# Kernel tuning notes

Hardware: AMD Instinct MI355X
Metric: run time of the kernel (lower is better)

The kernel has to match this reference:

```python
import jax, jax.numpy as jnp
import numpy as np

B, L, D, H = 4, 2048, 1024, 16
DH = D // H

def setup_inputs() -> dict:
    key = jax.random.key(0)
    ks = jax.random.split(key, 9)
    s = 1.0 / np.sqrt(D)
    x = jax.random.normal(ks[0], (B, L, D), dtype=jnp.float32)
    Wq = jax.random.uniform(ks[1], (D, D), jnp.float32, -s, s)
    bq = jax.random.uniform(ks[2], (D,), jnp.float32, -s, s)
    Wk = jax.random.uniform(ks[3], (D, D), jnp.float32, -s, s)
    bk = jax.random.uniform(ks[4], (D,), jnp.float32, -s, s)
    Wv = jax.random.uniform(ks[5], (D, D), jnp.float32, -s, s)
    bv = jax.random.uniform(ks[6], (D,), jnp.float32, -s, s)
    Wo = jax.random.uniform(ks[7], (D, D), jnp.float32, -s, s)
    bo = jax.random.uniform(ks[8], (D,), jnp.float32, -s, s)
    mask = jnp.tril(jnp.ones((L, L), dtype=jnp.int32))[None, None]  # [1,1,L,L] causal
    return {"x": x, "Wq": Wq, "bq": bq, "Wk": Wk, "bk": bk, "Wv": Wv, "bv": bv,
            "Wo": Wo, "bo": bo, "mask": mask}

def reference(x, Wq, bq, Wk, bk, Wv, bv, Wo, bo, mask):
    # projections (torch Linear: x @ W.T + b; here W stored transposed already as [D,D])
    q = (x @ Wq + bq).reshape(B, L, H, DH).transpose(0, 2, 1, 3)  # [B,H,L,Dh]
    k = (x @ Wk + bk).reshape(B, L, H, DH).transpose(0, 2, 1, 3)
    v = (x @ Wv + bv).reshape(B, L, H, DH).transpose(0, 2, 1, 3)
    scores = jnp.einsum('bhqd,bhkd->bhqk', q, k) / jnp.sqrt(jnp.float32(DH))
    scores = jnp.where(mask == 0, -jnp.inf, scores)
    attn = jax.nn.softmax(scores, axis=-1)
    out = jnp.einsum('bhqk,bhkd->bhqd', attn, v)  # [B,H,L,Dh]
    out = out.transpose(0, 2, 1, 3).reshape(B, L, D)
    return out @ Wo + bo
```

## Files before the change

### kernel.cpp

```cpp
#include <hip/hip_runtime.h>
#include <hip/hip_bf16.h>


typedef __bf16 bf16;
typedef __bf16 bf16x4 __attribute__((ext_vector_type(4)));
typedef __bf16 bf16x8 __attribute__((ext_vector_type(8)));
typedef float f32x4 __attribute__((ext_vector_type(4)));

#define DEV static __device__ __forceinline__

constexpr int B = 4, L = 2048, D = 1024, H = 16, DH = 64;
constexpr int BL = B * L;
constexpr int GM = 8192, GK = 1024;
constexpr int BKg = 64;

typedef __attribute__((address_space(1))) const void* gptr1;
typedef __attribute__((address_space(3))) void* lptr3;

DEV void load_lds16(const bf16* g, bf16* l) {
  __builtin_amdgcn_global_load_lds((gptr1)g, (lptr3)l, 16, 0, 0);
}

DEV f32x4 mfma(bf16x8 a, bf16x8 b, f32x4 c) {
  return __builtin_amdgcn_mfma_f32_16x16x32_bf16(a, b, c, 0, 0, 0);
}

DEV float scrub(float v) { return (v == v) ? v : 0.f; }

__global__ void sniff_k(const unsigned short* __restrict__ xr, int* flag) {
  __shared__ int cnt;
  if (threadIdx.x == 0) cnt = 0;
  __syncthreads();
  int local = 0;
  for (int i = threadIdx.x; i < 4096; i += 64) {
    const unsigned short u = xr[2 * i];
    const int e = (u >> 7) & 0xFF;
    if (e >= 0x70 && e <= 0x85) local++;
  }
  atomicAdd(&cnt, local);
  __syncthreads();
  if (threadIdx.x == 0) *flag = (cnt > 2048) ? 1 : 0;
}

__global__ __launch_bounds__(256) void cvt_x_k(const void* __restrict__ src,
                                               bf16* __restrict__ dst,
                                               const int* __restrict__ flag, int n) {
  const bool isbf = (*flag != 0);
  const int stride = gridDim.x * blockDim.x * 8;
  for (int idx = (blockIdx.x * blockDim.x + threadIdx.x) * 8; idx < n; idx += stride) {
    bf16x8 o;
    if (isbf) {
      bf16x8 v = *(const bf16x8*)((const bf16*)src + idx);
      #pragma unroll
      for (int j = 0; j < 8; ++j) o[j] = (bf16)scrub((float)v[j]);
    } else {
      const float* s = (const float*)src + idx;
      #pragma unroll
      for (int j = 0; j < 8; ++j) o[j] = (bf16)scrub(s[j]);
    }
    *(bf16x8*)&dst[idx] = o;
  }
}

__global__ __launch_bounds__(256) void wtrans_cvt4_k(const void* __restrict__ W0,
                                                     const void* __restrict__ W1,
                                                     const void* __restrict__ W2,
                                                     const void* __restrict__ W3,
                                                     bf16* __restrict__ dstBase,
                                                     const int* __restrict__ flag) {
  __shared__ bf16 t[32][33];
  const bool isbf = (*flag != 0);
  const int z = blockIdx.z;
  const void* src = (z == 0) ? W0 : (z == 1) ? W1 : (z == 2) ? W2 : W3;
  bf16* dst = dstBase + (size_t)z * D * D;
  const int bx = blockIdx.x * 32, by = blockIdx.y * 32;
  const int tx = threadIdx.x & 31, ty = threadIdx.x >> 5;
  for (int i = ty; i < 32; i += 8) {
    const size_t off = (size_t)(by + i) * D + bx + tx;
    const float v = isbf ? (float)((const bf16*)src)[off] : ((const float*)src)[off];
    t[i][tx] = (bf16)scrub(v);
  }
  __syncthreads();
  for (int i = ty; i < 32; i += 8)
    dst[(size_t)(bx + i) * D + by + tx] = t[tx][i];
}

__global__ __launch_bounds__(256) void vtrans_k(const bf16* __restrict__ V,
                                                bf16* __restrict__ VT) {
  __shared__ __align__(16) bf16 t[64 * 72];
  const int l0 = blockIdx.x * 64, bh = blockIdx.y;
  const int b = bh >> 4, h = bh & 15;
  const int tid = threadIdx.x;
  #pragma unroll
  for (int i = 0; i < 2; ++i) {
    const int o = tid * 8 + i * 2048;
    const int lrow = o >> 6, dcol = o & 63;
    *(bf16x8*)&t[lrow * 72 + dcol] =
        *(const bf16x8*)&V[(size_t)(b * L + l0 + lrow) * D + h * 64 + dcol];
  }
  __syncthreads();
  const int d = tid >> 2, kc = tid & 3;
  const int G = kc >> 1, hh = kc & 1;
  bf16x8 o0, o1;
  #pragma unroll
  for (int j = 0; j < 8; ++j) o0[j] = t[(kc * 16 + j) * 72 + d];
  #pragma unroll
  for (int j = 0; j < 8; ++j) o1[j] = t[(kc * 16 + 8 + j) * 72 + d];
  bf16* dst = VT + ((size_t)bh * DH + d) * L + l0 + G * 32;
  *(bf16x4*)(dst + hh * 4)      = __builtin_shufflevector(o0, o0, 0, 1, 2, 3);
  *(bf16x4*)(dst + 8 + hh * 4)  = __builtin_shufflevector(o0, o0, 4, 5, 6, 7);
  *(bf16x4*)(dst + 16 + hh * 4) = __builtin_shufflevector(o1, o1, 0, 1, 2, 3);
  *(bf16x4*)(dst + 24 + hh * 4) = __builtin_shufflevector(o1, o1, 4, 5, 6, 7);
}

__global__ __launch_bounds__(256) void qkv_gemm_k(const bf16* __restrict__ A,
                                                  const bf16* __restrict__ Bt,
                                                  const void* __restrict__ bq,
                                                  const void* __restrict__ bk,
                                                  const void* __restrict__ bv,
                                                  bf16* __restrict__ Q,
                                                  bf16* __restrict__ Kk,
                                                  bf16* __restrict__ V,
                                                  const int* __restrict__ flag) {
  __shared__ __align__(16) bf16 As[128 * BKg];
  __shared__ __align__(16) bf16 Bs[128 * BKg];
  const bool isbf = (*flag != 0);
  const int m0 = blockIdx.x * 128, n0 = blockIdx.y * 128;
  const int buf = n0 >> 10, nloc = n0 & 1023;
  bf16* Cb = (buf == 0) ? Q : (buf == 1) ? Kk : V;
  const void* bias = (buf == 0) ? bq : (buf == 1) ? bk : bv;
  const float scale = (buf == 0) ? 0.18033688011111f : 1.0f;

  const int tid = threadIdx.x, wave = tid >> 6, lane = tid & 63;
  const int wr = wave >> 1, wc = wave & 1;
  const int quad = lane >> 4, l16 = lane & 15;
  const int srow = lane >> 3;
  const int scol = ((lane ^ srow) & 7) * 8;
  const int l7 = l16 & 7;
  const int s0 = ((quad ^ l7) * 8);
  const int s1 = s0 ^ 32;

  f32x4 acc[4][4] = {};

  for (int k0 = 0; k0 < GK; k0 += BKg) {
    for (int c = wave; c < 16; c += 4) {
      load_lds16(A  + (size_t)(m0 + c * 8 + srow) * GK + k0 + scol, &As[c * 512]);
      load_lds16(Bt + (size_t)(n0 + c * 8 + srow) * GK + k0 + scol, &Bs[c * 512]);
    }
    __syncthreads();
    #pragma unroll
    for (int kk = 0; kk < BKg; kk += 32) {
      const int sk = kk ? s1 : s0;
      bf16x8 af[4], bfr[4];
      #pragma unroll
      for (int i = 0; i < 4; ++i)
        af[i] = *(const bf16x8*)&As[(wr * 64 + i * 16 + l16) * BKg + sk];
      #pragma unroll
      for (int i = 0; i < 4; ++i)
        bfr[i] = *(const bf16x8*)&Bs[(wc * 64 + i * 16 + l16) * BKg + sk];
      #pragma unroll
      for (int mi = 0; mi < 4; ++mi)
        #pragma unroll
        for (int ni = 0; ni < 4; ++ni)
          acc[mi][ni] = mfma(af[mi], bfr[ni], acc[mi][ni]);
    }
    __syncthreads();
  }

  #pragma unroll
  for (int ni = 0; ni < 4; ++ni) {
    const int col = nloc + wc * 64 + ni * 16 + l16;
    const float bv2 = isbf ? (float)((const bf16*)bias)[col] : ((const float*)bias)[col];
    #pragma unroll
    for (int mi = 0; mi < 4; ++mi)
      #pragma unroll
      for (int r = 0; r < 4; ++r) {
        const int row = m0 + wr * 64 + mi * 16 + quad * 4 + r;
        Cb[(size_t)row * D + col] = (bf16)((acc[mi][ni][r] + bv2) * scale);
      }
  }
}

__global__ __launch_bounds__(256) void gemm_bt_k(const bf16* __restrict__ A,
                                                 const bf16* __restrict__ Bt,
                                                 const void* __restrict__ bias,
                                                 void* __restrict__ C,
                                                 const int* __restrict__ flag) {
  __shared__ __align__(16) bf16 As[128 * BKg];
  __shared__ __align__(16) bf16 Bs[128 * BKg];
  const bool isbf = (*flag != 0);
  const int m0 = blockIdx.x * 128, n0 = blockIdx.y * 128;
  const int tid = threadIdx.x, wave = tid >> 6, lane = tid & 63;
  const int wr = wave >> 1, wc = wave & 1;
  const int quad = lane >> 4, l16 = lane & 15;
  const int srow = lane >> 3;
  const int scol = ((lane ^ srow) & 7) * 8;
  const int l7 = l16 & 7;
  const int s0 = ((quad ^ l7) * 8);
  const int s1 = s0 ^ 32;

  f32x4 acc[4][4] = {};

  for (int k0 = 0; k0 < GK; k0 += BKg) {
    for (int c = wave; c < 16; c += 4) {
      load_lds16(A  + (size_t)(m0 + c * 8 + srow) * GK + k0 + scol, &As[c * 512]);
      load_lds16(Bt + (size_t)(n0 + c * 8 + srow) * GK + k0 + scol, &Bs[c * 512]);
    }
    __syncthreads();
    #pragma unroll
    for (int kk = 0; kk < BKg; kk += 32) {
      const int sk = kk ? s1 : s0;
      bf16x8 af[4], bfr[4];
      #pragma unroll
      for (int i = 0; i < 4; ++i)
        af[i] = *(const bf16x8*)&As[(wr * 64 + i * 16 + l16) * BKg + sk];
      #pragma unroll
      for (int i = 0; i < 4; ++i)
        bfr[i] = *(const bf16x8*)&Bs[(wc * 64 + i * 16 + l16) * BKg + sk];
      #pragma unroll
      for (int mi = 0; mi < 4; ++mi)
        #pragma unroll
        for (int ni = 0; ni < 4; ++ni)
          acc[mi][ni] = mfma(af[mi], bfr[ni], acc[mi][ni]);
    }
    __syncthreads();
  }

  bf16* Cb = (bf16*)C;
  float* Cf = (float*)C;
  #pragma unroll
  for (int ni = 0; ni < 4; ++ni) {
    const int col = n0 + wc * 64 + ni * 16 + l16;
    const float bv = isbf ? (float)((const bf16*)bias)[col] : ((const float*)bias)[col];
    #pragma unroll
    for (int mi = 0; mi < 4; ++mi)
      #pragma unroll
      for (int r = 0; r < 4; ++r) {
        const int row = m0 + wr * 64 + mi * 16 + quad * 4 + r;
        const float v = acc[mi][ni][r] + bv;
        if (isbf) Cb[(size_t)row * D + col] = (bf16)v;
        else      Cf[(size_t)row * D + col] = v;
      }
  }
}

__global__ __launch_bounds__(256) void attn_k(bf16* QO,
                                              const bf16* __restrict__ K,
                                              const bf16* __restrict__ VT) {
  __shared__ __align__(16) bf16 Ks[2][64 * 64];
  __shared__ __align__(16) bf16 Vt[2][64 * 64];

  const int bx = blockIdx.x;
  const int qt = (L / 64 - 1) - (bx >> 6);
  const int bh = bx & 63;
  const int b = bh >> 4, h = bh & 15;
  const int tid = threadIdx.x, wave = tid >> 6, lane = tid & 63;
  const int quad = lane >> 4, l16 = lane & 15;
  const int srow = lane >> 3;
  const int scol = ((lane ^ srow) & 7) * 8;
  const int l7 = l16 & 7;
  const int s0 = ((quad ^ l7) * 8);
  const int s1 = s0 ^ 32;

  bf16* Qb = QO + (size_t)b * L * D + h * DH;
  const bf16* Kb = K + (size_t)b * L * D + h * DH;
  const bf16* VTg = VT + (size_t)bh * DH * L;

  const int qrow = qt * 64 + wave * 16 + l16;
  const bf16x8 qf0 = *(const bf16x8*)(Qb + (size_t)qrow * D + quad * 8);
  const bf16x8 qf1 = *(const bf16x8*)(Qb + (size_t)qrow * D + 32 + quad * 8);

  bf16x8 ones;
  #pragma unroll
  for (int j = 0; j < 8; ++j) ones[j] = (bf16)1.0f;

  float m_run = -INFINITY;
  f32x4 o_acc[4] = {};
  f32x4 o_sum = {};

  const int nkt = qt + 1;

  for (int c = wave; c < 8; c += 4) {
    load_lds16(Kb  + (size_t)(c * 8 + srow) * D + scol, &Ks[0][c * 512]);
    load_lds16(VTg + (size_t)(c * 8 + srow) * L + scol, &Vt[0][c * 512]);
  }
  __syncthreads();

  int cur = 0;
  for (int kt = 0; kt < nkt; ++kt) {
    if (kt + 1 < nkt) {
      for (int c = wave; c < 8; c += 4) {
        load_lds16(Kb  + (size_t)((kt + 1) * 64 + c * 8 + srow) * D + scol,
                   &Ks[cur ^ 1][c * 512]);
        load_lds16(VTg + (size_t)(c * 8 + srow) * L + (kt + 1) * 64 + scol,
                   &Vt[cur ^ 1][c * 512]);
      }
    }

    const bf16* Kc = &Ks[cur][0];
    const bf16* Vc = &Vt[cur][0];

    f32x4 s[4];
    #pragma unroll
    for (int sub = 0; sub < 4; ++sub) {
      bf16x8 k0 = *(const bf16x8*)&Kc[(sub * 16 + l16) * 64 + s0];
      bf16x8 k1 = *(const bf16x8*)&Kc[(sub * 16 + l16) * 64 + s1];
      f32x4 a = {};
      a = mfma(k0, qf0, a);
      a = mfma(k1, qf1, a);
      s[sub] = a;
    }

    if (kt == qt) {
      const int qloc = wave * 16 + l16;
      #pragma unroll
      for (int sub = 0; sub < 4; ++sub)
        #pragma unroll
        for (int r = 0; r < 4; ++r)
          if (sub * 16 + quad * 4 + r > qloc) s[sub][r] = -1e30f;
    }

    float mx = -INFINITY;
    #pragma unroll
    for (int sub = 0; sub < 4; ++sub) {
      const float a = fmaxf(fmaxf(s[sub][0], s[sub][1]), fmaxf(s[sub][2], s[sub][3]));
      mx = fmaxf(mx, a);
    }
    mx = fmaxf(mx, __shfl_xor(mx, 16, 64));
    mx = fmaxf(mx, __shfl_xor(mx, 32, 64));

    if (!__all(mx <= m_run + 8.f)) {
      const float mn = fmaxf(m_run, mx);
      const float alpha = __builtin_amdgcn_exp2f(m_run - mn);
      m_run = mn;
      #pragma unroll
      for (int r = 0; r < 4; ++r) {
        const float ar = __shfl(alpha, quad * 4 + r, 64);
        o_sum[r] *= ar;
        #pragma unroll
        for (int db = 0; db < 4; ++db) o_acc[db][r] *= ar;
      }
    }

    bf16x8 fr0, fr1;
    #pragma unroll
    for (int r = 0; r < 4; ++r) {
      fr0[r]     = (bf16)__builtin_amdgcn_exp2f(s[0][r] - m_run);
      fr0[4 + r] = (bf16)__builtin_amdgcn_exp2f(s[1][r] - m_run);
      fr1[r]     = (bf16)__builtin_amdgcn_exp2f(s[2][r] - m_run);
      fr1[4 + r] = (bf16)__builtin_amdgcn_exp2f(s[3][r] - m_run);
    }

    o_sum = mfma(fr0, ones, o_sum);
    o_sum = mfma(fr1, ones, o_sum);
    #pragma unroll
    for (int db = 0; db < 4; ++db) {
      bf16x8 v0 = *(const bf16x8*)&Vc[(db * 16 + l16) * 64 + s0];
      bf16x8 v1 = *(const bf16x8*)&Vc[(db * 16 + l16) * 64 + s1];
      o_acc[db] = mfma(fr0, v0, o_acc[db]);
      o_acc[db] = mfma(fr1, v1, o_acc[db]);
    }

    __syncthreads();
    cur ^= 1;
  }

  #pragma unroll
  for (int r = 0; r < 4; ++r) {
    const float inv = 1.f / o_sum[r];
    const int row = qt * 64 + wave * 16 + quad * 4 + r;
    #pragma unroll
    for (int db = 0; db < 4; ++db)
      Qb[(size_t)row * D + db * 16 + l16] = (bf16)(o_acc[db][r] * inv);
  }
}

extern "C" void kernel_launch(void* const* d_in, const int* in_sizes, int n_in,
                              void* d_out, int out_size, void* d_ws, size_t ws_size,
                              hipStream_t stream) {
  const void* x  = d_in[0];
  const void* Wq = d_in[1];
  const void* bq = d_in[2];
  const void* Wk = d_in[3];
  const void* bk = d_in[4];
  const void* Wv = d_in[5];
  const void* bv = d_in[6];
  const void* Wo = d_in[7];
  const void* bo = d_in[8];

  int* flag = (int*)d_ws;
  char* p = (char*)d_ws + 4096;
  bf16* xc  = (bf16*)p;                 p += (size_t)BL * D * 2;
  bf16* WqT = (bf16*)p;                 p += (size_t)D * D * 2;
  bf16* WkT = (bf16*)p;                 p += (size_t)D * D * 2;
  bf16* WvT = (bf16*)p;                 p += (size_t)D * D * 2;
  bf16* WoT = (bf16*)p;                 p += (size_t)D * D * 2;
  bf16* Qb  = (bf16*)p;                 p += (size_t)BL * D * 2;
  bf16* Kb  = (bf16*)p;                 p += (size_t)BL * D * 2;
  bf16* Vb  = (bf16*)p;
  bf16* VTb = xc;

  sniff_k<<<1, 64, 0, stream>>>((const unsigned short*)x, flag);

  cvt_x_k<<<1024, 256, 0, stream>>>(x, xc, flag, BL * D);
  wtrans_cvt4_k<<<dim3(32, 32, 4), 256, 0, stream>>>(Wq, Wk, Wv, Wo, WqT, flag);

  qkv_gemm_k<<<dim3(GM / 128, 3072 / 128), 256, 0, stream>>>(
      xc, WqT, bq, bk, bv, Qb, Kb, Vb, flag);

  vtrans_k<<<dim3(L / 64, B * H), 256, 0, stream>>>(Vb, VTb);

  attn_k<<<dim3((L / 64) * B * H), 256, 0, stream>>>(Qb, Kb, VTb);

  gemm_bt_k<<<dim3(GM / 128, D / 128), 256, 0, stream>>>(Qb, WoT, bo, d_out, flag);
}
```

Before: 300.0 us.

## Fuse V transpose into QKV GEMM epilogue and drop vtrans kernel

```diff
diff --git a/kernel.cpp b/kernel.cpp
--- a/kernel.cpp
+++ b/kernel.cpp
@@ -26,13 +26,14 @@
 }
 
 DEV float scrub(float v) { return (v == v) ? v : 0.f; }
+DEV float max3f(float a, float b, float c) { return fmaxf(fmaxf(a, b), c); }
 
 __global__ void sniff_k(const unsigned short* __restrict__ xr, int* flag) {
   __shared__ int cnt;
   if (threadIdx.x == 0) cnt = 0;
   __syncthreads();
   int local = 0;
-  for (int i = threadIdx.x; i < 4096; i += 64) {
+  for (int i = threadIdx.x; i < 4096; i += 256) {
     const unsigned short u = xr[2 * i];
     const int e = (u >> 7) & 0xFF;
     if (e >= 0x70 && e <= 0x85) local++;
@@ -85,34 +86,6 @@
     dst[(size_t)(bx + i) * D + by + tx] = t[tx][i];
 }
 
-__global__ __launch_bounds__(256) void vtrans_k(const bf16* __restrict__ V,
-                                                bf16* __restrict__ VT) {
-  __shared__ __align__(16) bf16 t[64 * 72];
-  const int l0 = blockIdx.x * 64, bh = blockIdx.y;
-  const int b = bh >> 4, h = bh & 15;
-  const int tid = threadIdx.x;
-  #pragma unroll
-  for (int i = 0; i < 2; ++i) {
-    const int o = tid * 8 + i * 2048;
-    const int lrow = o >> 6, dcol = o & 63;
-    *(bf16x8*)&t[lrow * 72 + dcol] =
-        *(const bf16x8*)&V[(size_t)(b * L + l0 + lrow) * D + h * 64 + dcol];
-  }
-  __syncthreads();
-  const int d = tid >> 2, kc = tid & 3;
-  const int G = kc >> 1, hh = kc & 1;
-  bf16x8 o0, o1;
-  #pragma unroll
-  for (int j = 0; j < 8; ++j) o0[j] = t[(kc * 16 + j) * 72 + d];
-  #pragma unroll
-  for (int j = 0; j < 8; ++j) o1[j] = t[(kc * 16 + 8 + j) * 72 + d];
-  bf16* dst = VT + ((size_t)bh * DH + d) * L + l0 + G * 32;
-  *(bf16x4*)(dst + hh * 4)      = __builtin_shufflevector(o0, o0, 0, 1, 2, 3);
-  *(bf16x4*)(dst + 8 + hh * 4)  = __builtin_shufflevector(o0, o0, 4, 5, 6, 7);
-  *(bf16x4*)(dst + 16 + hh * 4) = __builtin_shufflevector(o1, o1, 0, 1, 2, 3);
-  *(bf16x4*)(dst + 24 + hh * 4) = __builtin_shufflevector(o1, o1, 4, 5, 6, 7);
-}
-
 __global__ __launch_bounds__(256) void qkv_gemm_k(const bf16* __restrict__ A,
                                                   const bf16* __restrict__ Bt,
                                                   const void* __restrict__ bq,
@@ -120,14 +93,13 @@
                                                   const void* __restrict__ bv,
                                                   bf16* __restrict__ Q,
                                                   bf16* __restrict__ Kk,
-                                                  bf16* __restrict__ V,
+                                                  bf16* __restrict__ VT,
                                                   const int* __restrict__ flag) {
   __shared__ __align__(16) bf16 As[128 * BKg];
   __shared__ __align__(16) bf16 Bs[128 * BKg];
   const bool isbf = (*flag != 0);
   const int m0 = blockIdx.x * 128, n0 = blockIdx.y * 128;
   const int buf = n0 >> 10, nloc = n0 & 1023;
-  bf16* Cb = (buf == 0) ? Q : (buf == 1) ? Kk : V;
   const void* bias = (buf == 0) ? bq : (buf == 1) ? bk : bv;
   const float scale = (buf == 0) ? 0.18033688011111f : 1.0f;
 
@@ -167,17 +139,37 @@
     __syncthreads();
   }
 
-  #pragma unroll
-  for (int ni = 0; ni < 4; ++ni) {
-    const int col = nloc + wc * 64 + ni * 16 + l16;
-    const float bv2 = isbf ? (float)((const bf16*)bias)[col] : ((const float*)bias)[col];
-    #pragma unroll
-    for (int mi = 0; mi < 4; ++mi)
-      #pragma unroll
-      for (int r = 0; r < 4; ++r) {
-        const int row = m0 + wr * 64 + mi * 16 + quad * 4 + r;
-        Cb[(size_t)row * D + col] = (bf16)((acc[mi][ni][r] + bv2) * scale);
+  if (buf < 2) {
+    bf16* Cb = (buf == 0) ? Q : Kk;
+    #pragma unroll
+    for (int ni = 0; ni < 4; ++ni) {
+      const int col = nloc + wc * 64 + ni * 16 + l16;
+      const float bv2 = isbf ? (float)((const bf16*)bias)[col] : ((const float*)bias)[col];
+      #pragma unroll
+      for (int mi = 0; mi < 4; ++mi)
+        #pragma unroll
+        for (int r = 0; r < 4; ++r) {
+          const int row = m0 + wr * 64 + mi * 16 + quad * 4 + r;
+          Cb[(size_t)row * D + col] = (bf16)((acc[mi][ni][r] + bv2) * scale);
+        }
+    }
+  } else {
+    #pragma unroll
+    for (int ni = 0; ni < 4; ++ni) {
+      const int col = nloc + wc * 64 + ni * 16 + l16;
+      const int h = col >> 6, d = col & 63;
+      const float bv2 = isbf ? (float)((const bf16*)bias)[col] : ((const float*)bias)[col];
+      #pragma unroll
+      for (int mi = 0; mi < 4; ++mi) {
+        const int row = m0 + wr * 64 + mi * 16 + quad * 4;
+        const int bb = row >> 11, l = row & 2047;
+        const int pos = (l & ~31) + 4 * ((l >> 4) & 1) + 8 * ((l >> 2) & 3);
+        bf16x4 pk;
+        #pragma unroll
+        for (int r = 0; r < 4; ++r) pk[r] = (bf16)(acc[mi][ni][r] + bv2);
+        *(bf16x4*)&VT[((size_t)(bb * 16 + h) * 64 + d) * L + pos] = pk;
       }
+    }
   }
 }
 
@@ -320,12 +312,12 @@
           if (sub * 16 + quad * 4 + r > qloc) s[sub][r] = -1e30f;
     }
 
-    float mx = -INFINITY;
-    #pragma unroll
-    for (int sub = 0; sub < 4; ++sub) {
-      const float a = fmaxf(fmaxf(s[sub][0], s[sub][1]), fmaxf(s[sub][2], s[sub][3]));
-      mx = fmaxf(mx, a);
-    }
+    const float t0 = max3f(s[0][0], s[0][1], s[0][2]);
+    const float t1 = max3f(s[0][3], s[1][0], s[1][1]);
+    const float t2 = max3f(s[1][2], s[1][3], s[2][0]);
+    const float t3 = max3f(s[2][1], s[2][2], s[2][3]);
+    const float t4 = max3f(s[3][0], s[3][1], s[3][2]);
+    float mx = fmaxf(max3f(t0, t1, t2), max3f(t3, t4, s[3][3]));
     mx = fmaxf(mx, __shfl_xor(mx, 16, 64));
     mx = fmaxf(mx, __shfl_xor(mx, 32, 64));
 
@@ -397,18 +389,15 @@
   bf16* WoT = (bf16*)p;                 p += (size_t)D * D * 2;
   bf16* Qb  = (bf16*)p;                 p += (size_t)BL * D * 2;
   bf16* Kb  = (bf16*)p;                 p += (size_t)BL * D * 2;
-  bf16* Vb  = (bf16*)p;
-  bf16* VTb = xc;
-
-  sniff_k<<<1, 64, 0, stream>>>((const unsigned short*)x, flag);
+  bf16* VTb = (bf16*)p;
+
+  sniff_k<<<1, 256, 0, stream>>>((const unsigned short*)x, flag);
 
   cvt_x_k<<<1024, 256, 0, stream>>>(x, xc, flag, BL * D);
   wtrans_cvt4_k<<<dim3(32, 32, 4), 256, 0, stream>>>(Wq, Wk, Wv, Wo, WqT, flag);
 
   qkv_gemm_k<<<dim3(GM / 128, 3072 / 128), 256, 0, stream>>>(
-      xc, WqT, bq, bk, bv, Qb, Kb, Vb, flag);
-
-  vtrans_k<<<dim3(L / 64, B * H), 256, 0, stream>>>(Vb, VTb);
+      xc, WqT, bq, bk, bv, Qb, Kb, VTb, flag);
 
   attn_k<<<dim3((L / 64) * B * H), 256, 0, stream>>>(Qb, Kb, VTb);
 
```

After: 262.6 us. 1.14x faster.
